# Optimization experiments

Hardware: AMD Instinct MI355X
Metric: run time of the kernel (lower is better)

## Reference

```python
import jax, jax.numpy as jnp
import numpy as np

N_NODES = 100000
N_EDGES = 1000000
D_IN = 64
D_OUT = 64


def setup_inputs() -> dict:
    key = jax.random.key(0)
    k_x, k_e, k_w, k_b = jax.random.split(key, 4)
    x = jax.random.normal(k_x, (N_NODES, D_IN), dtype=jnp.float32)
    edge_index = jax.random.randint(k_e, (2, N_EDGES), 0, N_NODES, dtype=jnp.int64)
    # degrees of destination nodes (what the caller is expected to supply);
    # clamp to >=1 to avoid division by zero for isolated nodes
    deg = jax.ops.segment_sum(jnp.ones((N_EDGES,), jnp.float32), edge_index[1], num_segments=N_NODES)
    node_degrees = jnp.maximum(deg, 1.0)
    W = jax.random.normal(k_w, (D_OUT, D_IN), dtype=jnp.float32) * (1.0 / np.sqrt(D_IN))
    b = jax.random.normal(k_b, (D_OUT,), dtype=jnp.float32) * 0.01
    return {"x": x, "edge_index": edge_index, "node_degrees": node_degrees, "W": W, "b": b}


def reference(x, edge_index, node_degrees, W, b):
    # Original does argsort+cumsum+boundary segment-sum; mathematically this is
    # a scatter-add of gathered neighbor features into dst, i.e. a segment sum.
    src, dst = edge_index[0], edge_index[1]
    agg = jax.ops.segment_sum(x[src], dst, num_segments=x.shape[0])  # [N, D_IN]
    mean = agg / node_degrees[:, None]
    return mean @ W.T + b  # [N, D_OUT]
```

## Files before the change

kernel.cpp:

```cpp
#include <hip/hip_runtime.h>


#define D 64
#define BSHIFT 6
#define BNODES (1 << BSHIFT)
#define CAP 1024
#define GTHREADS 512
#define PERTHREAD (CAP / GTHREADS)
#define PXW_THREADS 512
#define MAXB 2048

__device__ inline int detect_stride_block(const unsigned* __restrict__ words,
                                          int E, int* sflag) {
    int t = threadIdx.x;
    if (t < 64) {
        unsigned v = (t < E) ? words[2 * t + 1] : 0u;
        int any = __any(v != 0u);
        if (t == 0) *sflag = any ? 1 : 2;
    }
    __syncthreads();
    return *sflag;
}

__device__ inline unsigned pack_bf16(float a, float b) {
    unsigned ua = __float_as_uint(a), ub = __float_as_uint(b);
    ua += 0x7fffu + ((ua >> 16) & 1u);
    ub += 0x7fffu + ((ub >> 16) & 1u);
    return (ua >> 16) | (ub & 0xffff0000u);
}

__global__ __launch_bounds__(PXW_THREADS, 4) void partition_xw_kernel(
        const unsigned* __restrict__ ewords, int* __restrict__ cursor,
        unsigned* __restrict__ pairs, uint2* __restrict__ spill,
        int* __restrict__ spillCnt,
        const float* __restrict__ x, const float* __restrict__ W,
        unsigned* __restrict__ y2, int E, int N, int nb, int pblocks) {
    __shared__ __align__(16) char smem[52240];
    int t = threadIdx.x;

    if ((int)blockIdx.x < pblocks) {
        int* lhist = (int*)smem;
        int* lbase = lhist + MAXB;
        int* sflag = lbase + MAXB;
        int s = detect_stride_block(ewords, E, sflag);
        int base = blockIdx.x * 8192;
        for (int i = t; i < nb; i += PXW_THREADS) lhist[i] = 0;
        __syncthreads();
        unsigned pv[16]; int bk[16];
        #pragma unroll
        for (int k = 0; k < 16; ++k) {
            int e = base + k * PXW_THREADS + t;
            bk[k] = -1;
            if (e < E) {
                unsigned src = ewords[(size_t)e * s];
                unsigned dst = ewords[((size_t)E + e) * s];
                bk[k] = (int)(dst >> BSHIFT);
                pv[k] = src | ((dst & (BNODES - 1)) << 17);
                atomicAdd(&lhist[bk[k]], 1);
            }
        }
        __syncthreads();
        for (int hb = t; hb < nb; hb += PXW_THREADS) {
            int cc = lhist[hb];
            if (cc) lbase[hb] = atomicAdd(&cursor[hb], cc);
            lhist[hb] = 0;
        }
        __syncthreads();
        #pragma unroll
        for (int k = 0; k < 16; ++k) {
            if (bk[k] >= 0) {
                int lpos = lbase[bk[k]] + atomicAdd(&lhist[bk[k]], 1);
                if (lpos < CAP) {
                    pairs[(size_t)bk[k] * CAP + lpos] = pv[k];
                } else {
                    int si = atomicAdd(spillCnt, 1);
                    unsigned dst = ((unsigned)bk[k] << BSHIFT) | (pv[k] >> 17);
                    spill[si] = make_uint2(pv[k] & 0x1FFFFu, dst);
                }
            }
        }
    } else {
        float* Wt = (float*)smem;
        float* xs = Wt + 64 * 68;
        for (int i = t; i < 64 * 64; i += PXW_THREADS) {
            int o = i >> 6, k = i & 63;
            Wt[k * 68 + o] = W[i];
        }
        int base = ((int)blockIdx.x - pblocks) * 128;
        int row = t >> 4, c4 = (t & 15) * 4;
        #pragma unroll
        for (int r = 0; r < 4; ++r) {
            int nl = row + r * 32;
            int n = base + nl;
            float4 v = {0.f, 0.f, 0.f, 0.f};
            if (n < N) v = *(const float4*)(x + (size_t)n * 64 + c4);
            *(float4*)&xs[nl * 68 + c4] = v;
        }
        __syncthreads();
        int o4 = (t & 15) * 4, nl4 = (t >> 4) * 4;
        float acc[4][4];
        #pragma unroll
        for (int i = 0; i < 4; ++i)
            #pragma unroll
            for (int j = 0; j < 4; ++j) acc[i][j] = 0.f;
        #pragma unroll 2
        for (int k0 = 0; k0 < 64; k0 += 4) {
            float a[4][4], wv[4][4];
            #pragma unroll
            for (int i = 0; i < 4; ++i)
                *(float4*)a[i] = *(const float4*)&xs[(nl4 + i) * 68 + k0];
            #pragma unroll
            for (int dk = 0; dk < 4; ++dk)
                *(float4*)wv[dk] = *(const float4*)&Wt[(k0 + dk) * 68 + o4];
            #pragma unroll
            for (int i = 0; i < 4; ++i)
                #pragma unroll
                for (int j = 0; j < 4; ++j)
                    acc[i][j] += a[i][0] * wv[0][j] + a[i][1] * wv[1][j]
                               + a[i][2] * wv[2][j] + a[i][3] * wv[3][j];
        }
        int n0 = base + nl4;
        #pragma unroll
        for (int i = 0; i < 4; ++i) {
            if (n0 + i < N) {
                uint2 p;
                p.x = pack_bf16(acc[i][0], acc[i][1]);
                p.y = pack_bf16(acc[i][2], acc[i][3]);
                *(uint2*)(y2 + (size_t)(n0 + i) * 32 + (o4 >> 1)) = p;
            }
        }
    }
}

#define RACC8(S, u) { \
    S[0] += __uint_as_float((u).x << 16); \
    S[1] += __uint_as_float((u).x & 0xffff0000u); \
    S[2] += __uint_as_float((u).y << 16); \
    S[3] += __uint_as_float((u).y & 0xffff0000u); \
    S[4] += __uint_as_float((u).z << 16); \
    S[5] += __uint_as_float((u).z & 0xffff0000u); \
    S[6] += __uint_as_float((u).w << 16); \
    S[7] += __uint_as_float((u).w & 0xffff0000u); }

__global__ __launch_bounds__(GTHREADS) void bucket_gather(
        const unsigned* __restrict__ y2, const unsigned* __restrict__ pairs,
        const int* __restrict__ cursor, const uint2* __restrict__ spill,
        const int* __restrict__ spillCnt,
        const float* __restrict__ deg, const float* __restrict__ b,
        float* __restrict__ out, int N) {
    __shared__ unsigned list[CAP];
    __shared__ int cnt[BNODES], st[BNODES], sc[BNODES];
    int t = threadIdx.x;
    int bkt = blockIdx.x, base = bkt << BSHIFT;
    int total = cursor[bkt];
    int cn = total < CAP ? total : CAP;
    int node = t >> 3, c = t & 7;
    float4 bv0 = ((const float4*)b)[c * 2];
    float4 bv1 = ((const float4*)b)[c * 2 + 1];

    if (t < BNODES) cnt[t] = 0;
    __syncthreads();
    unsigned pv[PERTHREAD];
    #pragma unroll
    for (int j = 0; j < PERTHREAD; ++j) {
        int i = t + j * GTHREADS;
        pv[j] = (i < cn) ? pairs[(size_t)bkt * CAP + i] : 0xFFFFFFFFu;
        if (pv[j] != 0xFFFFFFFFu) atomicAdd(&cnt[pv[j] >> 17], 1);
    }
    __syncthreads();
    if (t < 64) {
        int v = cnt[t];
        #pragma unroll
        for (int off = 1; off < 64; off <<= 1) {
            int u = __shfl_up(v, off);
            if (t >= off) v += u;
        }
        st[t] = v - cnt[t]; sc[t] = v - cnt[t];
    }
    __syncthreads();
    #pragma unroll
    for (int j = 0; j < PERTHREAD; ++j) {
        if (pv[j] != 0xFFFFFFFFu) {
            int pos = atomicAdd(&sc[pv[j] >> 17], 1);
            list[pos] = pv[j] & 0x1FFFFu;
        }
    }
    __syncthreads();

    int scnt = *spillCnt;

    int n = base + node;
    int s0 = st[node], e1 = s0 + cnt[node];
    float sa[8], sb[8], sc_[8], sd[8];
    #pragma unroll
    for (int k = 0; k < 8; ++k) { sa[k] = 0.f; sb[k] = 0.f; sc_[k] = 0.f; sd[k] = 0.f; }
    int i = s0;
    for (; i + 3 < e1; i += 4) {
        unsigned v0 = list[i], v1 = list[i + 1];
        unsigned v2 = list[i + 2], v3 = list[i + 3];
        uint4 u0 = *(const uint4*)(y2 + (size_t)v0 * 32 + c * 4);
        uint4 u1 = *(const uint4*)(y2 + (size_t)v1 * 32 + c * 4);
        uint4 u2 = *(const uint4*)(y2 + (size_t)v2 * 32 + c * 4);
        uint4 u3 = *(const uint4*)(y2 + (size_t)v3 * 32 + c * 4);
        RACC8(sa, u0);
        RACC8(sb, u1);
        RACC8(sc_, u2);
        RACC8(sd, u3);
    }
    if (i + 1 < e1) {
        unsigned v0 = list[i], v1 = list[i + 1];
        uint4 u0 = *(const uint4*)(y2 + (size_t)v0 * 32 + c * 4);
        uint4 u1 = *(const uint4*)(y2 + (size_t)v1 * 32 + c * 4);
        RACC8(sa, u0);
        RACC8(sb, u1);
        i += 2;
    }
    if (i < e1) {
        unsigned v0 = list[i];
        uint4 u0 = *(const uint4*)(y2 + (size_t)v0 * 32 + c * 4);
        RACC8(sa, u0);
    }
    #pragma unroll
    for (int k = 0; k < 8; ++k) sa[k] = (sa[k] + sb[k]) + (sc_[k] + sd[k]);
    for (int k = 0; k < scnt; ++k) {
        uint2 e = spill[k];
        if ((int)e.y == n) {
            uint4 u = *(const uint4*)(y2 + (size_t)e.x * 32 + c * 4);
            RACC8(sa, u);
        }
    }
    if (n < N) {
        float invd = 1.0f / deg[n];
        float4 o0 = {sa[0] * invd + bv0.x, sa[1] * invd + bv0.y,
                     sa[2] * invd + bv0.z, sa[3] * invd + bv0.w};
        float4 o1 = {sa[4] * invd + bv1.x, sa[5] * invd + bv1.y,
                     sa[6] * invd + bv1.z, sa[7] * invd + bv1.w};
        *(float4*)(out + (size_t)n * 64 + c * 8) = o0;
        *(float4*)(out + (size_t)n * 64 + c * 8 + 4) = o1;
    }
}

__global__ __launch_bounds__(256) void scatter_kernel(
        const float* __restrict__ x, const unsigned* __restrict__ ewords,
        float* __restrict__ agg, int E) {
    __shared__ int sflag;
    int s = detect_stride_block(ewords, E, &sflag);
    int gid = blockIdx.x * blockDim.x + threadIdx.x;
    int e = gid >> 4, q = gid & 15;
    if (e >= E) return;
    int src = (int)ewords[(size_t)e * s];
    int dst = (int)ewords[((size_t)E + e) * s];
    const float4 v = *(const float4*)(x + (size_t)src * D + q * 4);
    float* p = agg + (size_t)dst * D + q * 4;
    unsafeAtomicAdd(p + 0, v.x);
    unsafeAtomicAdd(p + 1, v.y);
    unsafeAtomicAdd(p + 2, v.z);
    unsafeAtomicAdd(p + 3, v.w);
}

__global__ __launch_bounds__(256) void gemm_kernel(
        float* __restrict__ inout, const float* __restrict__ deg,
        const float* __restrict__ W, const float* __restrict__ b, int nNodes) {
    __shared__ float Wt[64 * 65];
    __shared__ float rows[4 * 64];
    int t = threadIdx.x;
    for (int i = t; i < 64 * 64; i += 256) {
        int o = i >> 6, k = i & 63;
        Wt[k * 65 + o] = W[i];
    }
    int base = blockIdx.x * 4;
    int nl = t >> 6, o = t & 63;
    int n = base + nl;
    if (n < nNodes) {
        float invd = 1.0f / deg[n];
        rows[nl * 64 + o] = inout[(size_t)n * 64 + o] * invd;
    }
    __syncthreads();
    if (n >= nNodes) return;
    float acc = b[o];
    #pragma unroll
    for (int k = 0; k < 64; ++k)
        acc += rows[nl * 64 + k] * Wt[k * 65 + o];
    inout[(size_t)n * 64 + o] = acc;
}

extern "C" void kernel_launch(void* const* d_in, const int* in_sizes, int n_in,
                              void* d_out, int out_size, void* d_ws, size_t ws_size,
                              hipStream_t stream) {
    const float*    x      = (const float*)d_in[0];
    const unsigned* ewords = (const unsigned*)d_in[1];
    const float*    deg    = (const float*)d_in[2];
    const float*    W      = (const float*)d_in[3];
    const float*    b      = (const float*)d_in[4];
    float*          out    = (float*)d_out;

    const int E = in_sizes[1] / 2;
    const int N = in_sizes[2];
    const int nb = (N + BNODES - 1) >> BSHIFT;

    char* ws = (char*)d_ws;
    size_t curB  = (MAXB + 16) * 4;
    size_t pairB = ((size_t)nb * CAP * 4 + 63) & ~63ull;
    size_t spB   = ((size_t)E * 8 + 63) & ~63ull;
    size_t need  = curB + pairB + spB + (size_t)N * 32 * 4;

    if (ws_size >= need && N < (1 << 17) && nb <= MAXB) {
        int*      cursor   = (int*)ws;
        int*      spillCnt = cursor + MAXB;
        unsigned* pairs    = (unsigned*)(ws + curB);
        uint2*    spill    = (uint2*)(ws + curB + pairB);
        unsigned* y2       = (unsigned*)(ws + curB + pairB + spB);

        hipMemsetAsync(cursor, 0, curB, stream);

        int pblocks  = (E + 8191) / 8192;
        int xwblocks = (N + 127) / 128;
        partition_xw_kernel<<<pblocks + xwblocks, PXW_THREADS, 0, stream>>>(
            ewords, cursor, pairs, spill, spillCnt, x, W, y2, E, N, nb, pblocks);

        bucket_gather<<<nb, GTHREADS, 0, stream>>>(
            y2, pairs, cursor, spill, spillCnt, deg, b, out, N);
    } else {
        hipMemsetAsync(d_out, 0, (size_t)out_size * sizeof(float), stream);
        long long sthreads = (long long)E * 16;
        int sblocks = (int)((sthreads + 255) / 256);
        scatter_kernel<<<sblocks, 256, 0, stream>>>(x, ewords, out, E);
        gemm_kernel<<<(N + 3) / 4, 256, 0, stream>>>(out, deg, W, b, N);
    }
}
```

Measured before the change: 140.1 us.

## Compute x·Wᵀ projection with bf16 MFMA instead of FP32 LDS-tiled FMA

Replaces the shared-memory-tiled FP32 scalar GEMM in the projection blocks with bf16 MFMA 16x16x32 instructions. x and W fragments are loaded straight from global memory into registers and converted to bf16, so the W/x LDS staging and its barrier go away. This also shrinks the kernel's shared-memory allocation, which may raise occupancy for the partition blocks. In exchange, inputs are rounded to bf16 before the multiply rather than only at the output, and W is read repeatedly from global or cache by every wave.

```diff
diff --git a/kernel.cpp b/kernel.cpp
--- a/kernel.cpp
+++ b/kernel.cpp
@@ -10,6 +10,9 @@
 #define PXW_THREADS 512
 #define MAXB 2048
 
+typedef __attribute__((ext_vector_type(8))) short bf16x8;
+typedef __attribute__((ext_vector_type(4))) float f32x4;
+
 __device__ inline int detect_stride_block(const unsigned* __restrict__ words,
                                           int E, int* sflag) {
     int t = threadIdx.x;
@@ -29,13 +32,20 @@
     return (ua >> 16) | (ub & 0xffff0000u);
 }
 
+__device__ inline bf16x8 mk_frag(unsigned u0, unsigned u1,
+                                 unsigned u2, unsigned u3) {
+    union { unsigned u[4]; bf16x8 v; } r;
+    r.u[0] = u0; r.u[1] = u1; r.u[2] = u2; r.u[3] = u3;
+    return r.v;
+}
+
 __global__ __launch_bounds__(PXW_THREADS, 4) void partition_xw_kernel(
         const unsigned* __restrict__ ewords, int* __restrict__ cursor,
         unsigned* __restrict__ pairs, uint2* __restrict__ spill,
         int* __restrict__ spillCnt,
         const float* __restrict__ x, const float* __restrict__ W,
         unsigned* __restrict__ y2, int E, int N, int nb, int pblocks) {
-    __shared__ __align__(16) char smem[52240];
+    __shared__ __align__(16) char smem[16400];
     int t = threadIdx.x;
 
     if ((int)blockIdx.x < pblocks) {
@@ -80,54 +90,67 @@
             }
         }
     } else {
-        float* Wt = (float*)smem;
-        float* xs = Wt + 64 * 68;
-        for (int i = t; i < 64 * 64; i += PXW_THREADS) {
-            int o = i >> 6, k = i & 63;
-            Wt[k * 68 + o] = W[i];
-        }
+        int l = t & 63, w = t >> 6;
+        int rowi = l & 15, kq = l >> 4;
         int base = ((int)blockIdx.x - pblocks) * 128;
-        int row = t >> 4, c4 = (t & 15) * 4;
-        #pragma unroll
-        for (int r = 0; r < 4; ++r) {
-            int nl = row + r * 32;
-            int n = base + nl;
-            float4 v = {0.f, 0.f, 0.f, 0.f};
-            if (n < N) v = *(const float4*)(x + (size_t)n * 64 + c4);
-            *(float4*)&xs[nl * 68 + c4] = v;
-        }
-        __syncthreads();
-        int o4 = (t & 15) * 4, nl4 = (t >> 4) * 4;
-        float acc[4][4];
-        #pragma unroll
-        for (int i = 0; i < 4; ++i)
-            #pragma unroll
-            for (int j = 0; j < 4; ++j) acc[i][j] = 0.f;
-        #pragma unroll 2
-        for (int k0 = 0; k0 < 64; k0 += 4) {
-            float a[4][4], wv[4][4];
-            #pragma unroll
-            for (int i = 0; i < 4; ++i)
-                *(float4*)a[i] = *(const float4*)&xs[(nl4 + i) * 68 + k0];
-            #pragma unroll
-            for (int dk = 0; dk < 4; ++dk)
-                *(float4*)wv[dk] = *(const float4*)&Wt[(k0 + dk) * 68 + o4];
-            #pragma unroll
-            for (int i = 0; i < 4; ++i)
-                #pragma unroll
-                for (int j = 0; j < 4; ++j)
-                    acc[i][j] += a[i][0] * wv[0][j] + a[i][1] * wv[1][j]
-                               + a[i][2] * wv[2][j] + a[i][3] * wv[3][j];
-        }
-        int n0 = base + nl4;
-        #pragma unroll
-        for (int i = 0; i < 4; ++i) {
-            if (n0 + i < N) {
-                uint2 p;
-                p.x = pack_bf16(acc[i][0], acc[i][1]);
-                p.y = pack_bf16(acc[i][2], acc[i][3]);
-                *(uint2*)(y2 + (size_t)(n0 + i) * 32 + (o4 >> 1)) = p;
+        int n = base + w * 16 + rowi;
+        bf16x8 bfrag[2];
+        #pragma unroll
+        for (int kh = 0; kh < 2; ++kh) {
+            float4 f0 = {0.f, 0.f, 0.f, 0.f}, f1 = {0.f, 0.f, 0.f, 0.f};
+            if (n < N) {
+                const float* xp = x + (size_t)n * 64 + kh * 32 + kq * 8;
+                f0 = *(const float4*)xp;
+                f1 = *(const float4*)(xp + 4);
             }
+            bfrag[kh] = mk_frag(pack_bf16(f0.x, f0.y), pack_bf16(f0.z, f0.w),
+                                pack_bf16(f1.x, f1.y), pack_bf16(f1.z, f1.w));
+        }
+        f32x4 acc0 = {0.f, 0.f, 0.f, 0.f}, acc1 = acc0, acc2 = acc0, acc3 = acc0;
+        #pragma unroll
+        for (int kh = 0; kh < 2; ++kh) {
+            const float* wp = W + rowi * 64 + kh * 32 + kq * 8;
+            float4 g0, g1;
+            g0 = *(const float4*)(wp);
+            g1 = *(const float4*)(wp + 4);
+            acc0 = __builtin_amdgcn_mfma_f32_16x16x32_bf16(
+                mk_frag(pack_bf16(g0.x, g0.y), pack_bf16(g0.z, g0.w),
+                        pack_bf16(g1.x, g1.y), pack_bf16(g1.z, g1.w)),
+                bfrag[kh], acc0, 0, 0, 0);
+            g0 = *(const float4*)(wp + 16 * 64);
+            g1 = *(const float4*)(wp + 16 * 64 + 4);
+            acc1 = __builtin_amdgcn_mfma_f32_16x16x32_bf16(
+                mk_frag(pack_bf16(g0.x, g0.y), pack_bf16(g0.z, g0.w),
+                        pack_bf16(g1.x, g1.y), pack_bf16(g1.z, g1.w)),
+                bfrag[kh], acc1, 0, 0, 0);
+            g0 = *(const float4*)(wp + 32 * 64);
+            g1 = *(const float4*)(wp + 32 * 64 + 4);
+            acc2 = __builtin_amdgcn_mfma_f32_16x16x32_bf16(
+                mk_frag(pack_bf16(g0.x, g0.y), pack_bf16(g0.z, g0.w),
+                        pack_bf16(g1.x, g1.y), pack_bf16(g1.z, g1.w)),
+                bfrag[kh], acc2, 0, 0, 0);
+            g0 = *(const float4*)(wp + 48 * 64);
+            g1 = *(const float4*)(wp + 48 * 64 + 4);
+            acc3 = __builtin_amdgcn_mfma_f32_16x16x32_bf16(
+                mk_frag(pack_bf16(g0.x, g0.y), pack_bf16(g0.z, g0.w),
+                        pack_bf16(g1.x, g1.y), pack_bf16(g1.z, g1.w)),
+                bfrag[kh], acc3, 0, 0, 0);
+        }
+        if (n < N) {
+            unsigned* yp = y2 + (size_t)n * 32 + kq * 2;
+            uint2 p;
+            p.x = pack_bf16(acc0[0], acc0[1]);
+            p.y = pack_bf16(acc0[2], acc0[3]);
+            *(uint2*)(yp) = p;
+            p.x = pack_bf16(acc1[0], acc1[1]);
+            p.y = pack_bf16(acc1[2], acc1[3]);
+            *(uint2*)(yp + 8) = p;
+            p.x = pack_bf16(acc2[0], acc2[1]);
+            p.y = pack_bf16(acc2[2], acc2[3]);
+            *(uint2*)(yp + 16) = p;
+            p.x = pack_bf16(acc3[0], acc3[1]);
+            p.y = pack_bf16(acc3[2], acc3[3]);
+            *(uint2*)(yp + 24) = p;
         }
     }
 }
```

Result: no change. 142.2 us (+1.5%).
